# Kernel optimization log

Hardware: AMD Instinct MI355X
Metric: run time of the kernel (lower is better)

The kernel has to match this reference:

```python
import jax, jax.numpy as jnp
import numpy as np

EMBED_DIM = 64
NUM_EXPERTS = 4
SELECT_TOP_K = 2
N_TOKENS = 2097152


def setup_inputs() -> dict:
    key = jax.random.key(0)
    kx, kw = jax.random.split(key)
    x = jax.random.normal(kx, (N_TOKENS, EMBED_DIM), dtype=jnp.float32)
    # nn.Linear(64, 4, bias=False) weight: [out_features, in_features]
    W = jax.random.normal(kw, (NUM_EXPERTS, EMBED_DIM), dtype=jnp.float32) * (1.0 / np.sqrt(EMBED_DIM))
    return {"x": x, "W": W}


def reference(x, W):
    # logits: [N, E] = x @ W.T (Linear without bias)
    logits = jnp.einsum('nd,ed->ne', x, W)
    # top-k over experts
    topk_logits, topk_indices = jax.lax.top_k(logits, SELECT_TOP_K)  # [N, K]
    topk_probs = jax.nn.softmax(topk_logits, axis=-1)                # [N, K]
    # scatter top-k probs into dense [N, E] routing-weight tensor
    rows = jnp.arange(logits.shape[0])[:, None]                      # [N, 1]
    weights = jnp.zeros_like(logits).at[rows, topk_indices].set(topk_probs)
    return weights, topk_indices
```

## Files before the change

kernel.cpp:

```cpp
#include <hip/hip_runtime.h>
#include <math.h>

#define EMBED_DIM 64
#define NUM_EXPERTS 4
#define THREADS 128
#define TOK_PER_BLOCK 128
#define CHUNKS (TOK_PER_BLOCK * 16)

__global__ __launch_bounds__(THREADS) void gate_kernel(
    const float* __restrict__ x,
    const float* __restrict__ W,
    float* __restrict__ wout,
    float* __restrict__ iout,
    int n)
{
#pragma clang fp contract(off)
    __shared__ float4 lds[CHUNKS];

    const int t    = threadIdx.x;
    const int wave = t >> 6;
    const int lane = t & 63;
    const size_t blockChunk = (size_t)blockIdx.x * CHUNKS;

    const float4* x4 = reinterpret_cast<const float4*>(x);

    #pragma unroll
    for (int i = 0; i < 16; ++i) {
        const int base = (wave * 16 + i) * 64;
        const int L  = base + lane;
        const int tk = L >> 4;
        const int c  = L & 15;
        const int gc = (tk << 4) | (c ^ (tk & 7));
        __builtin_amdgcn_global_load_lds(
            (const __attribute__((address_space(1))) void*)(x4 + blockChunk + gc),
            (__attribute__((address_space(3))) void*)&lds[base],
            16, 0, 0);
    }
    __syncthreads();

    const float4* W4 = reinterpret_cast<const float4*>(W);

    float s0 = 0.0f, s1 = 0.0f, s2 = 0.0f, s3 = 0.0f;

    #pragma unroll
    for (int j = 0; j < 16; ++j) {
        const float4 xv = lds[(t << 4) | (j ^ (t & 7))];
        const float4 a = W4[0 * 16 + j];
        const float4 b = W4[1 * 16 + j];
        const float4 c = W4[2 * 16 + j];
        const float4 d = W4[3 * 16 + j];
        s0 = s0 + xv.x * a.x; s0 = s0 + xv.y * a.y;
        s0 = s0 + xv.z * a.z; s0 = s0 + xv.w * a.w;
        s1 = s1 + xv.x * b.x; s1 = s1 + xv.y * b.y;
        s1 = s1 + xv.z * b.z; s1 = s1 + xv.w * b.w;
        s2 = s2 + xv.x * c.x; s2 = s2 + xv.y * c.y;
        s2 = s2 + xv.z * c.z; s2 = s2 + xv.w * c.w;
        s3 = s3 + xv.x * d.x; s3 = s3 + xv.y * d.y;
        s3 = s3 + xv.z * d.z; s3 = s3 + xv.w * d.w;
    }

    int   i1 = 0;  float v1 = s0;
    if (s1 > v1) { v1 = s1; i1 = 1; }
    if (s2 > v1) { v1 = s2; i1 = 2; }
    if (s3 > v1) { v1 = s3; i1 = 3; }
    int   i2 = -1; float v2 = -INFINITY;
    if (i1 != 0 && s0 > v2) { v2 = s0; i2 = 0; }
    if (i1 != 1 && s1 > v2) { v2 = s1; i2 = 1; }
    if (i1 != 2 && s2 > v2) { v2 = s2; i2 = 2; }
    if (i1 != 3 && s3 > v2) { v2 = s3; i2 = 3; }

    const float e2  = expf(v2 - v1);
    const float den = 1.0f + e2;
    const float p1  = 1.0f / den;
    const float p2  = e2 / den;

    const int tok = blockIdx.x * TOK_PER_BLOCK + t;

    float4 wv;
    wv.x = (i1 == 0) ? p1 : ((i2 == 0) ? p2 : 0.0f);
    wv.y = (i1 == 1) ? p1 : ((i2 == 1) ? p2 : 0.0f);
    wv.z = (i1 == 2) ? p1 : ((i2 == 2) ? p2 : 0.0f);
    wv.w = (i1 == 3) ? p1 : ((i2 == 3) ? p2 : 0.0f);
    reinterpret_cast<float4*>(wout)[tok] = wv;

    float2 iv;
    iv.x = (float)i1;
    iv.y = (float)i2;
    reinterpret_cast<float2*>(iout)[tok] = iv;
}

extern "C" void kernel_launch(void* const* d_in, const int* in_sizes, int n_in,
                              void* d_out, int out_size, void* d_ws, size_t ws_size,
                              hipStream_t stream) {
    const float* x = (const float*)d_in[0];
    const float* W = (const float*)d_in[1];
    const int n = in_sizes[0] / EMBED_DIM;

    float* wout = (float*)d_out;
    float* iout = wout + (size_t)n * NUM_EXPERTS;

    const int grid = n / TOK_PER_BLOCK;
    hipLaunchKernelGGL(gate_kernel, dim3(grid), dim3(THREADS), 0, stream,
                       x, W, wout, iout, n);
}
```

Baseline: 116.5 us.

## Convert gate kernel to persistent per-wave tile loop without block barriers

Replaces the one-shot grid of 128-token blocks with a fixed grid of 1280 persistent blocks in which each wave independently loops over 64-token tiles. Each wave loads its own tile into a private LDS region and waits with s_waitcnt vmcnt(0) instead of a __syncthreads, which removes block-level synchronisation and per-block launch overhead. The risk is that each wave serialises load then compute with no double buffering, so memory latency is exposed on every iteration. Fewer resident waves may also lower achieved bandwidth compared with the many-block launch.

```diff
diff --git a/kernel.cpp b/kernel.cpp
--- a/kernel.cpp
+++ b/kernel.cpp
@@ -4,8 +4,8 @@
 #define EMBED_DIM 64
 #define NUM_EXPERTS 4
 #define THREADS 128
-#define TOK_PER_BLOCK 128
-#define CHUNKS (TOK_PER_BLOCK * 16)
+#define TILE_CHUNKS 1024
+#define NBLOCKS 1280
 
 __global__ __launch_bounds__(THREADS) void gate_kernel(
     const float* __restrict__ x,
@@ -15,78 +15,82 @@
     int n)
 {
 #pragma clang fp contract(off)
-    __shared__ float4 lds[CHUNKS];
+    __shared__ float4 lds[2 * TILE_CHUNKS];
 
-    const int t    = threadIdx.x;
-    const int wave = t >> 6;
-    const int lane = t & 63;
-    const size_t blockChunk = (size_t)blockIdx.x * CHUNKS;
+    const int lane = threadIdx.x & 63;
+    const int wid  = threadIdx.x >> 6;
+    const int gw   = blockIdx.x * 2 + wid;
+    const int nw   = NBLOCKS * 2;
+    const int ntiles = n / 64;
 
     const float4* x4 = reinterpret_cast<const float4*>(x);
+    const float4* W4 = reinterpret_cast<const float4*>(W);
+    float4* tilebuf = &lds[wid * TILE_CHUNKS];
 
-    #pragma unroll
-    for (int i = 0; i < 16; ++i) {
-        const int base = (wave * 16 + i) * 64;
-        const int L  = base + lane;
-        const int tk = L >> 4;
-        const int c  = L & 15;
-        const int gc = (tk << 4) | (c ^ (tk & 7));
-        __builtin_amdgcn_global_load_lds(
-            (const __attribute__((address_space(1))) void*)(x4 + blockChunk + gc),
-            (__attribute__((address_space(3))) void*)&lds[base],
-            16, 0, 0);
+    for (int t = gw; t < ntiles; t += nw) {
+        const size_t tileChunk = (size_t)t * TILE_CHUNKS;
+
+        #pragma unroll
+        for (int i = 0; i < 16; ++i) {
+            const int L  = i * 64 + lane;
+            const int tk = L >> 4;
+            const int c  = L & 15;
+            const int gc = (tk << 4) | (c ^ (tk & 7));
+            __builtin_amdgcn_global_load_lds(
+                (const __attribute__((address_space(1))) void*)(x4 + tileChunk + gc),
+                (__attribute__((address_space(3))) void*)&tilebuf[i * 64],
+                16, 0, 0);
+        }
+        asm volatile("s_waitcnt vmcnt(0)" ::: "memory");
+        __builtin_amdgcn_sched_barrier(0);
+
+        float s0 = 0.0f, s1 = 0.0f, s2 = 0.0f, s3 = 0.0f;
+        #pragma unroll
+        for (int j = 0; j < 16; ++j) {
+            const float4 xv = tilebuf[(lane << 4) | (j ^ (lane & 7))];
+            const float4 a = W4[ 0 + j];
+            const float4 b = W4[16 + j];
+            const float4 c = W4[32 + j];
+            const float4 d = W4[48 + j];
+            s0 = s0 + xv.x * a.x; s0 = s0 + xv.y * a.y;
+            s0 = s0 + xv.z * a.z; s0 = s0 + xv.w * a.w;
+            s1 = s1 + xv.x * b.x; s1 = s1 + xv.y * b.y;
+            s1 = s1 + xv.z * b.z; s1 = s1 + xv.w * b.w;
+            s2 = s2 + xv.x * c.x; s2 = s2 + xv.y * c.y;
+            s2 = s2 + xv.z * c.z; s2 = s2 + xv.w * c.w;
+            s3 = s3 + xv.x * d.x; s3 = s3 + xv.y * d.y;
+            s3 = s3 + xv.z * d.z; s3 = s3 + xv.w * d.w;
+        }
+
+        int   i1 = 0;  float v1 = s0;
+        if (s1 > v1) { v1 = s1; i1 = 1; }
+        if (s2 > v1) { v1 = s2; i1 = 2; }
+        if (s3 > v1) { v1 = s3; i1 = 3; }
+        int   i2 = -1; float v2 = -INFINITY;
+        if (i1 != 0 && s0 > v2) { v2 = s0; i2 = 0; }
+        if (i1 != 1 && s1 > v2) { v2 = s1; i2 = 1; }
+        if (i1 != 2 && s2 > v2) { v2 = s2; i2 = 2; }
+        if (i1 != 3 && s3 > v2) { v2 = s3; i2 = 3; }
+
+        const float e2  = expf(v2 - v1);
+        const float den = 1.0f + e2;
+        const float p1  = 1.0f / den;
+        const float p2  = e2 / den;
+
+        const int tok = t * 64 + lane;
+
+        float4 wv;
+        wv.x = (i1 == 0) ? p1 : ((i2 == 0) ? p2 : 0.0f);
+        wv.y = (i1 == 1) ? p1 : ((i2 == 1) ? p2 : 0.0f);
+        wv.z = (i1 == 2) ? p1 : ((i2 == 2) ? p2 : 0.0f);
+        wv.w = (i1 == 3) ? p1 : ((i2 == 3) ? p2 : 0.0f);
+        reinterpret_cast<float4*>(wout)[tok] = wv;
+
+        float2 iv;
+        iv.x = (float)i1;
+        iv.y = (float)i2;
+        reinterpret_cast<float2*>(iout)[tok] = iv;
     }
-    __syncthreads();
-
-    const float4* W4 = reinterpret_cast<const float4*>(W);
-
-    float s0 = 0.0f, s1 = 0.0f, s2 = 0.0f, s3 = 0.0f;
-
-    #pragma unroll
-    for (int j = 0; j < 16; ++j) {
-        const float4 xv = lds[(t << 4) | (j ^ (t & 7))];
-        const float4 a = W4[0 * 16 + j];
-        const float4 b = W4[1 * 16 + j];
-        const float4 c = W4[2 * 16 + j];
-        const float4 d = W4[3 * 16 + j];
-        s0 = s0 + xv.x * a.x; s0 = s0 + xv.y * a.y;
-        s0 = s0 + xv.z * a.z; s0 = s0 + xv.w * a.w;
-        s1 = s1 + xv.x * b.x; s1 = s1 + xv.y * b.y;
-        s1 = s1 + xv.z * b.z; s1 = s1 + xv.w * b.w;
-        s2 = s2 + xv.x * c.x; s2 = s2 + xv.y * c.y;
-        s2 = s2 + xv.z * c.z; s2 = s2 + xv.w * c.w;
-        s3 = s3 + xv.x * d.x; s3 = s3 + xv.y * d.y;
-        s3 = s3 + xv.z * d.z; s3 = s3 + xv.w * d.w;
-    }
-
-    int   i1 = 0;  float v1 = s0;
-    if (s1 > v1) { v1 = s1; i1 = 1; }
-    if (s2 > v1) { v1 = s2; i1 = 2; }
-    if (s3 > v1) { v1 = s3; i1 = 3; }
-    int   i2 = -1; float v2 = -INFINITY;
-    if (i1 != 0 && s0 > v2) { v2 = s0; i2 = 0; }
-    if (i1 != 1 && s1 > v2) { v2 = s1; i2 = 1; }
-    if (i1 != 2 && s2 > v2) { v2 = s2; i2 = 2; }
-    if (i1 != 3 && s3 > v2) { v2 = s3; i2 = 3; }
-
-    const float e2  = expf(v2 - v1);
-    const float den = 1.0f + e2;
-    const float p1  = 1.0f / den;
-    const float p2  = e2 / den;
-
-    const int tok = blockIdx.x * TOK_PER_BLOCK + t;
-
-    float4 wv;
-    wv.x = (i1 == 0) ? p1 : ((i2 == 0) ? p2 : 0.0f);
-    wv.y = (i1 == 1) ? p1 : ((i2 == 1) ? p2 : 0.0f);
-    wv.z = (i1 == 2) ? p1 : ((i2 == 2) ? p2 : 0.0f);
-    wv.w = (i1 == 3) ? p1 : ((i2 == 3) ? p2 : 0.0f);
-    reinterpret_cast<float4*>(wout)[tok] = wv;
-
-    float2 iv;
-    iv.x = (float)i1;
-    iv.y = (float)i2;
-    reinterpret_cast<float2*>(iout)[tok] = iv;
 }
 
 extern "C" void kernel_launch(void* const* d_in, const int* in_sizes, int n_in,
@@ -99,7 +103,6 @@
     float* wout = (float*)d_out;
     float* iout = wout + (size_t)n * NUM_EXPERTS;
 
-    const int grid = n / TOK_PER_BLOCK;
-    hipLaunchKernelGGL(gate_kernel, dim3(grid), dim3(THREADS), 0, stream,
+    hipLaunchKernelGGL(gate_kernel, dim3(NBLOCKS), dim3(THREADS), 0, stream,
                        x, W, wout, iout, n);
 }
```

New measurement: 127.7 us. 1.1x slower.
